# Performance work log

Hardware: AMD Instinct MI355X
Metric: run time of the kernel (lower is better)

Reference implementation:

```python
import jax, jax.numpy as jnp
import numpy as np
from jax.scipy.special import logsumexp

EPS = 0.02     # entropic regularization for approximate OT (mimics approximate EMD CUDA kernel)
ITERS = 20     # fixed Sinkhorn iterations


def _approx_emd(x, y):
    """Entropy-regularized optimal transport cost between equal-size point sets.
    x, y: [B, N, 3]. Returns per-batch cost summed over points (matching the
    CUDA earth_mover_distance convention of summing matched squared distances)."""
    # squared Euclidean cost matrix [B, N, N]
    C = jnp.sum((x[:, :, None, :] - y[:, None, :, :]) ** 2, axis=-1)
    B, N, M = C.shape
    logmu = jnp.float32(-np.log(N))   # uniform source marginal (log)
    lognu = jnp.float32(-np.log(M))   # uniform target marginal (log)

    def body(carry, _):
        f, g = carry  # dual potentials [B,N], [B,M]
        f = EPS * (logmu - logsumexp((g[:, None, :] - C) / EPS, axis=2))
        g = EPS * (lognu - logsumexp((f[:, :, None] - C) / EPS, axis=1))
        return (f, g), None

    f0 = jnp.zeros((B, N), dtype=C.dtype)
    g0 = jnp.zeros((B, M), dtype=C.dtype)
    (f, g), _ = jax.lax.scan(body, (f0, g0), None, length=ITERS)

    # transport plan in log-domain: logP_ij = (f_i + g_j - C_ij)/eps + logmu + lognu
    logP = (f[:, :, None] + g[:, None, :] - C) / EPS + logmu + lognu
    cost = jnp.sum(jnp.exp(logP) * C, axis=(1, 2))  # mean-normalized transport cost
    return cost * N  # sum over points, like the CUDA kernel


def setup_inputs() -> dict:
    key = jax.random.key(0)
    k1, k2 = jax.random.split(key)
    array1 = jax.random.normal(k1, (16, 2048, 3), dtype=jnp.float32)
    array2 = jax.random.normal(k2, (16, 2048, 3), dtype=jnp.float32)
    return {"array1": array1, "array2": array2}


def reference(array1, array2):
    num_point = array1.shape[1]
    emd = _approx_emd(array1, array2)  # [B]
    return 10.0 * jnp.mean(emd) / num_point
```

## Files before the change

### kernel.cpp

```cpp
#include <hip/hip_runtime.h>


namespace {
constexpr int BATCH = 16;
constexpr int NPT   = 2048;
constexpr int BLOCKS_PER_BATCH = 32;
constexpr int ROWS_PER_BLOCK   = 64;
constexpr int NSLICE = 4;
constexpr int JSLICE = NPT / NSLICE;
constexpr int NBLOCKS  = BATCH * BLOCKS_PER_BATCH;
constexpr int NTHREADS = ROWS_PER_BLOCK * NSLICE;
constexpr int ITERS = 20;
constexpr int CHUNK = 16;

constexpr int BAR_STRIDE = 32;
constexpr int BAR_BYTES  = 4096;

constexpr float SCL     = 72.13475204444817f;
constexpr float TWOS    = 144.26950408889634f;
constexpr float UCONST  = -11.0f;
constexpr float Q_CONST = -22.0f;

__device__ inline float fexp2(float x) { return __builtin_amdgcn_exp2f(x); }

struct Smem {
  float4 tab[NSLICE * JSLICE];
  float  redM[NSLICE * ROWS_PER_BLOCK];
  float  redS[NSLICE * ROWS_PER_BLOCK];
  float  wsum[NTHREADS / 64];
};

__device__ inline void arrive_and_wait(unsigned* bar, unsigned target, int tid) {
  __syncthreads();
  if (tid == 0) {
    __hip_atomic_fetch_add(bar, 1u, __ATOMIC_RELEASE, __HIP_MEMORY_SCOPE_AGENT);
    while (__hip_atomic_load(bar, __ATOMIC_ACQUIRE, __HIP_MEMORY_SCOPE_AGENT) < target) {}
  }
  __syncthreads();
}

__device__ inline void half_phase(float p0, float p1, float p2,
                                  const float4* __restrict__ T,
                                  float4* __restrict__ outT,
                                  Smem& sm,
                                  int batch, int row, int slice, int lane, int tid) {
  {
    const float4* __restrict__ gsrc = T + (size_t)batch * NPT + slice * JSLICE;
    float4* __restrict__ ldst = sm.tab + slice * JSLICE;
#pragma unroll
    for (int k = 0; k < JSLICE / 64; ++k)
      ldst[k * 64 + lane] = gsrc[k * 64 + lane];
  }
  __syncthreads();

  const float a0 = p0 * TWOS, a1 = p1 * TWOS, a2 = p2 * TWOS;
  const float4* __restrict__ tb = sm.tab + slice * JSLICE;

  float m = -3.0e38f;
  float s0 = 0.f, s1 = 0.f;
  for (int c = 0; c < JSLICE; c += CHUNK) {
    float z[CHUNK];
#pragma unroll
    for (int k = 0; k < CHUNK; ++k) {
      float4 t = tb[c + k];
      z[k] = fmaf(a0, t.x, fmaf(a1, t.y, fmaf(a2, t.z, t.w)));
    }
    float m0 = fmaxf(fmaxf(z[0],  z[1]),  z[2]);
    float m1 = fmaxf(fmaxf(z[3],  z[4]),  z[5]);
    float m2 = fmaxf(fmaxf(z[6],  z[7]),  z[8]);
    float m3 = fmaxf(fmaxf(z[9],  z[10]), z[11]);
    float m4 = fmaxf(fmaxf(z[12], z[13]), z[14]);
    float mn = fmaxf(fmaxf(fmaxf(m0, m1), m2), fmaxf(fmaxf(m3, m4), z[15]));
    float mN = fmaxf(m, mn);
    float r = fexp2(m - mN);
    s0 *= r; s1 *= r;
    m = mN;
#pragma unroll
    for (int k = 0; k < CHUNK; k += 2) {
      s0 += fexp2(z[k] - m);
      s1 += fexp2(z[k + 1] - m);
    }
  }

  sm.redM[slice * ROWS_PER_BLOCK + lane] = m;
  sm.redS[slice * ROWS_PER_BLOCK + lane] = s0 + s1;
  __syncthreads();
  if (tid < ROWS_PER_BLOCK) {
    float M = sm.redM[tid], S = sm.redS[tid];
#pragma unroll
    for (int q = 1; q < NSLICE; ++q) {
      float m2q = sm.redM[q * ROWS_PER_BLOCK + tid];
      float s2q = sm.redS[q * ROWS_PER_BLOCK + tid];
      float Mn = fmaxf(M, m2q);
      S = fmaf(S, fexp2(M - Mn), s2q * fexp2(m2q - Mn));
      M = Mn;
    }
    float u = UCONST - (M + __log2f(S));
    outT[batch * NPT + row] = make_float4(p0, p1, p2, u);
  }
}

__global__ __launch_bounds__(NTHREADS, 2)
void sinkhorn_emd_kernel(const float* __restrict__ X, const float* __restrict__ Y,
                         float* __restrict__ ws, float* __restrict__ out) {
  unsigned* __restrict__ bars = (unsigned*)ws;
  float4* tF = (float4*)((char*)ws + BAR_BYTES);
  float4* tG = tF + BATCH * NPT;

  const int tid  = threadIdx.x;
  const int bid  = blockIdx.x;
  const int gtid = bid * NTHREADS + tid;

  __shared__ Smem sm;

  if (gtid < BATCH * NPT) {
    const float* yp = Y + (size_t)gtid * 3;
    float y0 = yp[0], y1 = yp[1], y2 = yp[2];
    float yy = fmaf(y0, y0, fmaf(y1, y1, y2 * y2));
    tF[gtid] = make_float4(y0, y1, y2, -yy * SCL);
  }
  if (gtid == 0) out[0] = 0.f;

  const int xcd   = bid & 7;
  const int slot  = bid >> 3;
  const int batch = xcd * 2 + (slot >> 5);
  const int rb    = slot & (BLOCKS_PER_BATCH - 1);
  const int lane  = tid & (ROWS_PER_BLOCK - 1);
  const int slice = tid >> 6;
  const int row   = rb * ROWS_PER_BLOCK + lane;
  const int rowIdx = batch * NPT + row;

  const float* xp = X + (size_t)rowIdx * 3;
  const float px0 = xp[0], px1 = xp[1], px2 = xp[2];
  const float* yp2 = Y + (size_t)rowIdx * 3;
  const float py0 = yp2[0], py1 = yp2[1], py2 = yp2[2];

  arrive_and_wait(bars + 512, NBLOCKS, tid);

  unsigned* __restrict__ bar = bars + batch * BAR_STRIDE;
  unsigned targ = BLOCKS_PER_BATCH;

  for (int it = 0; it < ITERS; ++it) {
    half_phase(px0, px1, px2, tF, tG, sm, batch, row, slice, lane, tid);
    arrive_and_wait(bar, targ, tid); targ += BLOCKS_PER_BATCH;
    half_phase(py0, py1, py2, tG, tF, sm, batch, row, slice, lane, tid);
    arrive_and_wait(bar, targ, tid); targ += BLOCKS_PER_BATCH;
  }

  {
    {
      const float4* __restrict__ gsrc = tF + (size_t)batch * NPT + slice * JSLICE;
      float4* __restrict__ ldst = sm.tab + slice * JSLICE;
#pragma unroll
      for (int k = 0; k < JSLICE / 64; ++k)
        ldst[k * 64 + lane] = gsrc[k * 64 + lane];
    }
    __syncthreads();

    const float nrm = fmaf(px0, px0, fmaf(px1, px1, px2 * px2));
    const float q = tG[rowIdx].w + Q_CONST;
    const float4* __restrict__ tb = sm.tab + slice * JSLICE;
    float acc = 0.f;
    for (int c = 0; c < JSLICE; c += 4) {
#pragma unroll
      for (int k = 0; k < 4; ++k) {
        float4 t = tb[c + k];
        float dot = fmaf(px2, t.z, fmaf(px1, t.y, px0 * t.x));
        float yy  = fmaf(t.z, t.z, fmaf(t.y, t.y, t.x * t.x));
        float Cij = fmaf(-2.f, dot, nrm + yy);
        float lp  = fmaf(TWOS, dot, q + t.w);
        acc = fmaf(fexp2(lp), Cij, acc);
      }
    }
    for (int off = 32; off; off >>= 1) acc += __shfl_down(acc, off, 64);
    if ((tid & 63) == 0) sm.wsum[tid >> 6] = acc;
    __syncthreads();
    if (tid == 0) {
      float tot = 0.f;
#pragma unroll
      for (int k = 0; k < NTHREADS / 64; ++k) tot += sm.wsum[k];
      atomicAdd(out, 0.625f * tot);
    }
  }
}
}

extern "C" void kernel_launch(void* const* d_in, const int* in_sizes, int n_in,
                              void* d_out, int out_size, void* d_ws, size_t ws_size,
                              hipStream_t stream) {
  const float* X = (const float*)d_in[0];
  const float* Y = (const float*)d_in[1];
  float* out = (float*)d_out;
  float* ws  = (float*)d_ws;

  hipMemsetAsync(ws, 0, BAR_BYTES, stream);

  void* args[] = {(void*)&X, (void*)&Y, (void*)&ws, (void*)&out};
  hipLaunchCooperativeKernel((const void*)sinkhorn_emd_kernel,
                             dim3(NBLOCKS), dim3(NTHREADS),
                             args, 0, stream);
}
```

Baseline: 1.280 ms.

## Process two rows per thread to halve blocks and reuse LDS table reads

Each thread now handles two rows (A and B) per half-phase, so every float4 loaded from shared memory is reused for two logsumexp accumulations. Blocks per batch drop from 32 to 16, which halves the grid-barrier participants and the global-to-LDS table copies per iteration. The cost is higher register pressure (launch bounds lowered to 1 block per CU) and fewer blocks, so there is less latency hiding and less parallelism across CUs.

Measured after the change: 1.399 ms. +9.3%, slower.

```diff
diff --git a/kernel.cpp b/kernel.cpp
--- a/kernel.cpp
+++ b/kernel.cpp
@@ -4,12 +4,12 @@
 namespace {
 constexpr int BATCH = 16;
 constexpr int NPT   = 2048;
-constexpr int BLOCKS_PER_BATCH = 32;
-constexpr int ROWS_PER_BLOCK   = 64;
+constexpr int BLOCKS_PER_BATCH = 16;
+constexpr int ROWS_PER_BLOCK   = 128;
 constexpr int NSLICE = 4;
 constexpr int JSLICE = NPT / NSLICE;
 constexpr int NBLOCKS  = BATCH * BLOCKS_PER_BATCH;
-constexpr int NTHREADS = ROWS_PER_BLOCK * NSLICE;
+constexpr int NTHREADS = 256;
 constexpr int ITERS = 20;
 constexpr int CHUNK = 16;
 
@@ -24,10 +24,10 @@
 __device__ inline float fexp2(float x) { return __builtin_amdgcn_exp2f(x); }
 
 struct Smem {
-  float4 tab[NSLICE * JSLICE];
+  float4 tab[NPT];
   float  redM[NSLICE * ROWS_PER_BLOCK];
   float  redS[NSLICE * ROWS_PER_BLOCK];
-  float  wsum[NTHREADS / 64];
+  float  wsum[4];
 };
 
 __device__ inline void arrive_and_wait(unsigned* bar, unsigned target, int tid) {
@@ -39,11 +39,30 @@
   __syncthreads();
 }
 
-__device__ inline void half_phase(float p0, float p1, float p2,
+__device__ inline void lse_chunk(const float (&z)[CHUNK], float& m, float& s0, float& s1) {
+  float m0 = fmaxf(fmaxf(z[0],  z[1]),  z[2]);
+  float m1 = fmaxf(fmaxf(z[3],  z[4]),  z[5]);
+  float m2 = fmaxf(fmaxf(z[6],  z[7]),  z[8]);
+  float m3 = fmaxf(fmaxf(z[9],  z[10]), z[11]);
+  float m4 = fmaxf(fmaxf(z[12], z[13]), z[14]);
+  float mn = fmaxf(fmaxf(fmaxf(m0, m1), m2), fmaxf(fmaxf(m3, m4), z[15]));
+  float mN = fmaxf(m, mn);
+  float r = fexp2(m - mN);
+  s0 *= r; s1 *= r;
+  m = mN;
+#pragma unroll
+  for (int k = 0; k < CHUNK; k += 2) {
+    s0 += fexp2(z[k] - m);
+    s1 += fexp2(z[k + 1] - m);
+  }
+}
+
+__device__ inline void half_phase(float pA0, float pA1, float pA2,
+                                  float pB0, float pB1, float pB2,
                                   const float4* __restrict__ T,
                                   float4* __restrict__ outT,
                                   Smem& sm,
-                                  int batch, int row, int slice, int lane, int tid) {
+                                  int batch, int rowBase, int slice, int lane, int tid) {
   {
     const float4* __restrict__ gsrc = T + (size_t)batch * NPT + slice * JSLICE;
     float4* __restrict__ ldst = sm.tab + slice * JSLICE;
@@ -53,37 +72,28 @@
   }
   __syncthreads();
 
-  const float a0 = p0 * TWOS, a1 = p1 * TWOS, a2 = p2 * TWOS;
+  const float aA0 = pA0 * TWOS, aA1 = pA1 * TWOS, aA2 = pA2 * TWOS;
+  const float aB0 = pB0 * TWOS, aB1 = pB1 * TWOS, aB2 = pB2 * TWOS;
   const float4* __restrict__ tb = sm.tab + slice * JSLICE;
 
-  float m = -3.0e38f;
-  float s0 = 0.f, s1 = 0.f;
+  float mA = -3.0e38f, sA0 = 0.f, sA1 = 0.f;
+  float mB = -3.0e38f, sB0 = 0.f, sB1 = 0.f;
   for (int c = 0; c < JSLICE; c += CHUNK) {
-    float z[CHUNK];
+    float zA[CHUNK], zB[CHUNK];
 #pragma unroll
     for (int k = 0; k < CHUNK; ++k) {
       float4 t = tb[c + k];
-      z[k] = fmaf(a0, t.x, fmaf(a1, t.y, fmaf(a2, t.z, t.w)));
+      zA[k] = fmaf(aA0, t.x, fmaf(aA1, t.y, fmaf(aA2, t.z, t.w)));
+      zB[k] = fmaf(aB0, t.x, fmaf(aB1, t.y, fmaf(aB2, t.z, t.w)));
     }
-    float m0 = fmaxf(fmaxf(z[0],  z[1]),  z[2]);
-    float m1 = fmaxf(fmaxf(z[3],  z[4]),  z[5]);
-    float m2 = fmaxf(fmaxf(z[6],  z[7]),  z[8]);
-    float m3 = fmaxf(fmaxf(z[9],  z[10]), z[11]);
-    float m4 = fmaxf(fmaxf(z[12], z[13]), z[14]);
-    float mn = fmaxf(fmaxf(fmaxf(m0, m1), m2), fmaxf(fmaxf(m3, m4), z[15]));
-    float mN = fmaxf(m, mn);
-    float r = fexp2(m - mN);
-    s0 *= r; s1 *= r;
-    m = mN;
-#pragma unroll
-    for (int k = 0; k < CHUNK; k += 2) {
-      s0 += fexp2(z[k] - m);
-      s1 += fexp2(z[k + 1] - m);
-    }
-  }
-
-  sm.redM[slice * ROWS_PER_BLOCK + lane] = m;
-  sm.redS[slice * ROWS_PER_BLOCK + lane] = s0 + s1;
+    lse_chunk(zA, mA, sA0, sA1);
+    lse_chunk(zB, mB, sB0, sB1);
+  }
+
+  sm.redM[slice * ROWS_PER_BLOCK + lane] = mA;
+  sm.redS[slice * ROWS_PER_BLOCK + lane] = sA0 + sA1;
+  sm.redM[slice * ROWS_PER_BLOCK + 64 + lane] = mB;
+  sm.redS[slice * ROWS_PER_BLOCK + 64 + lane] = sB0 + sB1;
   __syncthreads();
   if (tid < ROWS_PER_BLOCK) {
     float M = sm.redM[tid], S = sm.redS[tid];
@@ -96,11 +106,14 @@
       M = Mn;
     }
     float u = UCONST - (M + __log2f(S));
-    outT[batch * NPT + row] = make_float4(p0, p1, p2, u);
-  }
-}
-
-__global__ __launch_bounds__(NTHREADS, 2)
+    float w0 = (tid < 64) ? pA0 : pB0;
+    float w1 = (tid < 64) ? pA1 : pB1;
+    float w2 = (tid < 64) ? pA2 : pB2;
+    outT[batch * NPT + rowBase + tid] = make_float4(w0, w1, w2, u);
+  }
+}
+
+__global__ __launch_bounds__(NTHREADS, 1)
 void sinkhorn_emd_kernel(const float* __restrict__ X, const float* __restrict__ Y,
                          float* __restrict__ ws, float* __restrict__ out) {
   unsigned* __restrict__ bars = (unsigned*)ws;
@@ -123,17 +136,22 @@
 
   const int xcd   = bid & 7;
   const int slot  = bid >> 3;
-  const int batch = xcd * 2 + (slot >> 5);
+  const int batch = xcd * 2 + (slot >> 4);
   const int rb    = slot & (BLOCKS_PER_BATCH - 1);
-  const int lane  = tid & (ROWS_PER_BLOCK - 1);
+  const int lane  = tid & 63;
   const int slice = tid >> 6;
-  const int row   = rb * ROWS_PER_BLOCK + lane;
-  const int rowIdx = batch * NPT + row;
-
-  const float* xp = X + (size_t)rowIdx * 3;
-  const float px0 = xp[0], px1 = xp[1], px2 = xp[2];
-  const float* yp2 = Y + (size_t)rowIdx * 3;
-  const float py0 = yp2[0], py1 = yp2[1], py2 = yp2[2];
+  const int rowBase = rb * ROWS_PER_BLOCK;
+  const int rowA  = rowBase + lane;
+  const int rowB  = rowA + 64;
+
+  const float* xa = X + (size_t)(batch * NPT + rowA) * 3;
+  const float pxA0 = xa[0], pxA1 = xa[1], pxA2 = xa[2];
+  const float* xb = X + (size_t)(batch * NPT + rowB) * 3;
+  const float pxB0 = xb[0], pxB1 = xb[1], pxB2 = xb[2];
+  const float* ya = Y + (size_t)(batch * NPT + rowA) * 3;
+  const float pyA0 = ya[0], pyA1 = ya[1], pyA2 = ya[2];
+  const float* yb = Y + (size_t)(batch * NPT + rowB) * 3;
+  const float pyB0 = yb[0], pyB1 = yb[1], pyB2 = yb[2];
 
   arrive_and_wait(bars + 512, NBLOCKS, tid);
 
@@ -141,9 +159,11 @@
   unsigned targ = BLOCKS_PER_BATCH;
 
   for (int it = 0; it < ITERS; ++it) {
-    half_phase(px0, px1, px2, tF, tG, sm, batch, row, slice, lane, tid);
+    half_phase(pxA0, pxA1, pxA2, pxB0, pxB1, pxB2, tF, tG, sm,
+               batch, rowBase, slice, lane, tid);
     arrive_and_wait(bar, targ, tid); targ += BLOCKS_PER_BATCH;
-    half_phase(py0, py1, py2, tG, tF, sm, batch, row, slice, lane, tid);
+    half_phase(pyA0, pyA1, pyA2, pyB0, pyB1, pyB2, tG, tF, sm,
+               batch, rowBase, slice, lane, tid);
     arrive_and_wait(bar, targ, tid); targ += BLOCKS_PER_BATCH;
   }
 
@@ -157,30 +177,37 @@
     }
     __syncthreads();
 
-    const float nrm = fmaf(px0, px0, fmaf(px1, px1, px2 * px2));
-    const float q = tG[rowIdx].w + Q_CONST;
     const float4* __restrict__ tb = sm.tab + slice * JSLICE;
-    float acc = 0.f;
-    for (int c = 0; c < JSLICE; c += 4) {
-#pragma unroll
-      for (int k = 0; k < 4; ++k) {
-        float4 t = tb[c + k];
-        float dot = fmaf(px2, t.z, fmaf(px1, t.y, px0 * t.x));
-        float yy  = fmaf(t.z, t.z, fmaf(t.y, t.y, t.x * t.x));
-        float Cij = fmaf(-2.f, dot, nrm + yy);
-        float lp  = fmaf(TWOS, dot, q + t.w);
-        acc = fmaf(fexp2(lp), Cij, acc);
+
+    auto final_sub = [&](float p0, float p1, float p2, int rowH) {
+      const float nrm = fmaf(p0, p0, fmaf(p1, p1, p2 * p2));
+      const float q = tG[batch * NPT + rowH].w + Q_CONST;
+      float acc = 0.f;
+      for (int c = 0; c < JSLICE; c += 4) {
+#pragma unroll
+        for (int k = 0; k < 4; ++k) {
+          float4 t = tb[c + k];
+          float dot = fmaf(p2, t.z, fmaf(p1, t.y, p0 * t.x));
+          float yy  = fmaf(t.z, t.z, fmaf(t.y, t.y, t.x * t.x));
+          float Cij = fmaf(-2.f, dot, nrm + yy);
+          float lp  = fmaf(TWOS, dot, q + t.w);
+          acc = fmaf(fexp2(lp), Cij, acc);
+        }
       }
-    }
-    for (int off = 32; off; off >>= 1) acc += __shfl_down(acc, off, 64);
-    if ((tid & 63) == 0) sm.wsum[tid >> 6] = acc;
-    __syncthreads();
-    if (tid == 0) {
-      float tot = 0.f;
-#pragma unroll
-      for (int k = 0; k < NTHREADS / 64; ++k) tot += sm.wsum[k];
-      atomicAdd(out, 0.625f * tot);
-    }
+      for (int off = 32; off; off >>= 1) acc += __shfl_down(acc, off, 64);
+      if ((tid & 63) == 0) sm.wsum[tid >> 6] = acc;
+      __syncthreads();
+      if (tid == 0) {
+        float tot = 0.f;
+#pragma unroll
+        for (int k = 0; k < 4; ++k) tot += sm.wsum[k];
+        atomicAdd(out, 0.625f * tot);
+      }
+      __syncthreads();
+    };
+
+    final_sub(pxA0, pxA1, pxA2, rowBase + lane);
+    final_sub(pxB0, pxB1, pxB2, rowBase + 64 + lane);
   }
 }
 }
```
